# Performance work log

Measured on AMD Instinct MI355X. Metric: run time of the kernel, lower is better.

The kernel has to match this reference:

```python
import jax, jax.numpy as jnp
import numpy as np

D_MODEL = 1024
N_HEADS = 16
HEAD_DIM = D_MODEL // N_HEADS
SEQ_LEN = 2048
D_FF = 4 * D_MODEL
LCC_SCALE = 0.1
LN_EPS = 1e-5
NORM_EPS = 1e-12  # F.normalize eps


def _layer_norm(x, g, b):
    mu = jnp.mean(x, axis=-1, keepdims=True)
    var = jnp.mean(jnp.square(x - mu), axis=-1, keepdims=True)
    return (x - mu) * jax.lax.rsqrt(var + LN_EPS) * g + b


def setup_inputs() -> dict:
    key = jax.random.key(0)
    ks = jax.random.split(key, 8)
    s = 0.02  # weight init scale
    return {
        "x": jax.random.normal(ks[0], (SEQ_LEN, D_MODEL), jnp.float32),
        "lcc_values": jax.random.uniform(ks[1], (SEQ_LEN,), jnp.float32),
        "w_qkv": jax.random.normal(ks[2], (D_MODEL, 3 * D_MODEL), jnp.float32) * s,
        "b_qkv": jnp.zeros((3 * D_MODEL,), jnp.float32),
        "w_out": jax.random.normal(ks[3], (D_MODEL, D_MODEL), jnp.float32) * s,
        "b_out": jnp.zeros((D_MODEL,), jnp.float32),
        "ln1_g": jnp.ones((D_MODEL,), jnp.float32),
        "ln1_b": jnp.zeros((D_MODEL,), jnp.float32),
        "ln2_g": jnp.ones((D_MODEL,), jnp.float32),
        "ln2_b": jnp.zeros((D_MODEL,), jnp.float32),
        "w_ff1": jax.random.normal(ks[4], (D_MODEL, D_FF), jnp.float32) * s,
        "b_ff1": jnp.zeros((D_FF,), jnp.float32),
        "w_ff2": jax.random.normal(ks[5], (D_FF, D_MODEL), jnp.float32) * s,
        "b_ff2": jnp.zeros((D_MODEL,), jnp.float32),
    }


def reference(x, lcc_values, w_qkv, b_qkv, w_out, b_out, ln1_g, ln1_b,
              ln2_g, ln2_b, w_ff1, b_ff1, w_ff2, b_ff2):
    L = x.shape[0]
    scaling = HEAD_DIM ** -0.5

    normed = _layer_norm(x, ln1_g, ln1_b)
    qkv = normed @ w_qkv + b_qkv                      # [L, 3D]
    qkv = qkv.reshape(L, 3, N_HEADS, HEAD_DIM)
    q = jnp.transpose(qkv[:, 0], (1, 0, 2))           # [H, L, d]
    k = jnp.transpose(qkv[:, 1], (1, 0, 2))
    v = jnp.transpose(qkv[:, 2], (1, 0, 2))

    # cosine attention: L2-normalize q, k
    q = q / jnp.maximum(jnp.linalg.norm(q, axis=-1, keepdims=True), NORM_EPS)
    k = k / jnp.maximum(jnp.linalg.norm(k, axis=-1, keepdims=True), NORM_EPS)
    q = q * scaling

    scores = jnp.einsum('hld,hmd->hlm', q, k)         # [H, L, L]
    bias = (lcc_values[:, None] + lcc_values[None, :]) * 0.5 * LCC_SCALE
    scores = jnp.clip(scores + bias[None], -10.0, 10.0)
    probs = jax.nn.softmax(scores, axis=-1)

    attn = jnp.einsum('hlm,hmd->hld', probs, v)       # [H, L, d]
    attn = jnp.transpose(attn, (1, 0, 2)).reshape(L, D_MODEL)
    x = x + (attn @ w_out + b_out)

    normed2 = _layer_norm(x, ln2_g, ln2_b)
    h = jax.nn.gelu(normed2 @ w_ff1 + b_ff1, approximate=False)
    x = x + (h @ w_ff2 + b_ff2)
    return x
```

## Files before the change

### kernel.cpp

```cpp
#include <hip/hip_runtime.h>
#include <hip/hip_bf16.h>

#define D_MODEL 1024
#define SEQ 2048
#define NH 16
#define HD 64
#define DFF 4096

typedef __attribute__((ext_vector_type(8))) __bf16 bf16x8;
typedef __attribute__((ext_vector_type(4))) float f32x4;

__device__ __forceinline__ unsigned short f2bf(float f) {
    union { float f; unsigned u; } v; v.f = f;
    unsigned r = v.u + 0x7fffu + ((v.u >> 16) & 1u);
    return (unsigned short)(r >> 16);
}
__device__ __forceinline__ unsigned pack2(float a, float b) {
    return (unsigned)f2bf(a) | ((unsigned)f2bf(b) << 16);
}
__device__ __forceinline__ float bf2f(unsigned short u) {
    union { unsigned u; float f; } v; v.u = ((unsigned)u) << 16;
    return v.f;
}
__device__ __forceinline__ bf16x8 ld_frag(const unsigned short* p) {
    union { uint4 u; bf16x8 b; } c;
    c.u = *(const uint4*)p;
    return c.b;
}

typedef __attribute__((address_space(3))) unsigned lds_u32;
typedef const __attribute__((address_space(1))) unsigned glob_u32;
__device__ __forceinline__ void gl_lds16(const unsigned short* g, unsigned short* l) {
    __builtin_amdgcn_global_load_lds((glob_u32*)g, (lds_u32*)l, 16, 0, 0);
}

#define MFMA16(a,b,c) __builtin_amdgcn_mfma_f32_16x16x32_bf16(a,b,c,0,0,0)

__global__ __launch_bounds__(256) void wcast_all(const float* __restrict__ wq, const float* __restrict__ wo,
                                                 const float* __restrict__ wf1, const float* __restrict__ wf2,
                                                 unsigned short* __restrict__ oq, unsigned short* __restrict__ oo,
                                                 unsigned short* __restrict__ of1, unsigned short* __restrict__ of2) {
    __shared__ unsigned short lt[64][72];
    int id = blockIdx.x;
    const float* W; unsigned short* O; int K, N, nb, kb;
    if (id < 768)       { W = wq;  O = oq;  K = 1024; N = 3072; nb = id % 48; kb = id / 48; }
    else if (id < 1024) { id -= 768;  W = wo;  O = oo;  K = 1024; N = 1024; nb = id & 15; kb = id >> 4; }
    else if (id < 2048) { id -= 1024; W = wf1; O = of1; K = 1024; N = 4096; nb = id & 63; kb = id >> 6; }
    else                { id -= 2048; W = wf2; O = of2; K = 4096; N = 1024; nb = id & 15; kb = id >> 4; }
    int t = threadIdx.x;
    int r = t >> 2, c0 = (t & 3) << 4;
    const float* src = W + (size_t)(kb*64 + r) * N + nb*64 + c0;
    float4 f0 = ((const float4*)src)[0];
    float4 f1 = ((const float4*)src)[1];
    float4 f2 = ((const float4*)src)[2];
    float4 f3 = ((const float4*)src)[3];
    unsigned* dst = (unsigned*)&lt[r][c0];
    dst[0]=pack2(f0.x,f0.y); dst[1]=pack2(f0.z,f0.w);
    dst[2]=pack2(f1.x,f1.y); dst[3]=pack2(f1.z,f1.w);
    dst[4]=pack2(f2.x,f2.y); dst[5]=pack2(f2.z,f2.w);
    dst[6]=pack2(f3.x,f3.y); dst[7]=pack2(f3.z,f3.w);
    __syncthreads();
    int n_ = t >> 2, k0 = (t & 3) << 4;
    unsigned obuf[8];
#pragma unroll
    for (int i = 0; i < 8; i++)
        obuf[i] = (unsigned)lt[k0 + 2*i][n_] | ((unsigned)lt[k0 + 2*i + 1][n_] << 16);
    unsigned short* out = O + (size_t)(nb*64 + n_) * K + kb*64 + k0;
    ((uint4*)out)[0] = *(uint4*)&obuf[0];
    ((uint4*)out)[1] = *(uint4*)&obuf[4];
}

__global__ __launch_bounds__(256) void ln_kernel(const float* __restrict__ x,
                                                 const float* __restrict__ g,
                                                 const float* __restrict__ b,
                                                 unsigned short* __restrict__ out) {
    int row = blockIdx.x, t = threadIdx.x;
    float4 v = ((const float4*)(x + (size_t)row * D_MODEL))[t];
    float s  = v.x + v.y + v.z + v.w;
    float sq = v.x*v.x + v.y*v.y + v.z*v.z + v.w*v.w;
#pragma unroll
    for (int m = 1; m < 64; m <<= 1) { s += __shfl_xor(s, m, 64); sq += __shfl_xor(sq, m, 64); }
    __shared__ float ls[4], lq[4];
    int wave = t >> 6, lane = t & 63;
    if (lane == 0) { ls[wave] = s; lq[wave] = sq; }
    __syncthreads();
    s  = ls[0]+ls[1]+ls[2]+ls[3];
    sq = lq[0]+lq[1]+lq[2]+lq[3];
    float mu  = s * (1.0f / D_MODEL);
    float var = sq * (1.0f / D_MODEL) - mu * mu;
    float rs  = rsqrtf(var + 1e-5f);
    int c = t * 4;
    float y0 = (v.x - mu) * rs * g[c+0] + b[c+0];
    float y1 = (v.y - mu) * rs * g[c+1] + b[c+1];
    float y2 = (v.z - mu) * rs * g[c+2] + b[c+2];
    float y3 = (v.w - mu) * rs * g[c+3] + b[c+3];
    unsigned* o = (unsigned*)(out + (size_t)row * D_MODEL + c);
    o[0] = pack2(y0, y1); o[1] = pack2(y2, y3);
}

__global__ __launch_bounds__(256) void reduce_ln(const float* __restrict__ x,
                                                 const float* __restrict__ bout,
                                                 const unsigned short* __restrict__ parts,
                                                 const float* __restrict__ g,
                                                 const float* __restrict__ b,
                                                 float* __restrict__ x1,
                                                 unsigned short* __restrict__ x2n) {
    int row = blockIdx.x, t = threadIdx.x;
    int i = row * 256 + t;
    float4 v = ((const float4*)x)[i];
    float4 bb = ((const float4*)bout)[t];
    v.x += bb.x; v.y += bb.y; v.z += bb.z; v.w += bb.w;
    ushort4 u0 = ((const ushort4*)parts)[i];
    ushort4 u1 = ((const ushort4*)(parts + (size_t)SEQ*D_MODEL))[i];
    v.x += bf2f(u0.x) + bf2f(u1.x);
    v.y += bf2f(u0.y) + bf2f(u1.y);
    v.z += bf2f(u0.z) + bf2f(u1.z);
    v.w += bf2f(u0.w) + bf2f(u1.w);
    ((float4*)x1)[i] = v;
    float s  = v.x + v.y + v.z + v.w;
    float sq = v.x*v.x + v.y*v.y + v.z*v.z + v.w*v.w;
#pragma unroll
    for (int m = 1; m < 64; m <<= 1) { s += __shfl_xor(s, m, 64); sq += __shfl_xor(sq, m, 64); }
    __shared__ float ls[4], lq[4];
    int wave = t >> 6, lane = t & 63;
    if (lane == 0) { ls[wave] = s; lq[wave] = sq; }
    __syncthreads();
    s  = ls[0]+ls[1]+ls[2]+ls[3];
    sq = lq[0]+lq[1]+lq[2]+lq[3];
    float mu  = s * (1.0f / D_MODEL);
    float var = sq * (1.0f / D_MODEL) - mu * mu;
    float rs  = rsqrtf(var + 1e-5f);
    int c = t * 4;
    float y0 = (v.x - mu) * rs * g[c+0] + b[c+0];
    float y1 = (v.y - mu) * rs * g[c+1] + b[c+1];
    float y2 = (v.z - mu) * rs * g[c+2] + b[c+2];
    float y3 = (v.w - mu) * rs * g[c+3] + b[c+3];
    unsigned* o = (unsigned*)(x2n + (size_t)row * D_MODEL + c);
    o[0] = pack2(y0, y1); o[1] = pack2(y2, y3);
}

__global__ __launch_bounds__(256) void reduce_ff2(const float* __restrict__ res,
                                                  const float* __restrict__ bias,
                                                  const unsigned short* __restrict__ parts,
                                                  float* __restrict__ out) {
    int i = blockIdx.x * 256 + threadIdx.x;
    float4 r = ((const float4*)res)[i];
    float4 b = ((const float4*)bias)[i & (D_MODEL/4 - 1)];
    r.x += b.x; r.y += b.y; r.z += b.z; r.w += b.w;
#pragma unroll
    for (int p = 0; p < 4; p++) {
        ushort4 u = ((const ushort4*)(parts + (size_t)p * SEQ * D_MODEL))[i];
        r.x += bf2f(u.x); r.y += bf2f(u.y); r.z += bf2f(u.z); r.w += bf2f(u.w);
    }
    ((float4*)out)[i] = r;
}

#define TMg 128
#define TNg 128
#define SMEM_U16 (2 * (TMg + TNg) * 64)
__device__ __forceinline__ void gemm_core(const unsigned short* __restrict__ A,
                                          const unsigned short* __restrict__ Bt,
                                          int K, int K0, int KS, int bm, int bn,
                                          unsigned short* smem, f32x4 acc[4][4],
                                          int wave, int lane) {
    constexpr int AI = 4, BI = 4, MI = 4, NI = 4;
    constexpr int HALF = (TMg + TNg) * 64;
    int quad = lane >> 4, lr = lane & 15;

    const unsigned short* pa[AI];
    int aoff[AI];
#pragma unroll
    for (int i = 0; i < AI; i++) {
        int rl = wave*32 + i*8 + (lane >> 3);
        int ss = (lane & 7) ^ (rl & 7);
        pa[i] = A + (size_t)(bm*TMg + rl) * K + K0 + ss*8;
        aoff[i] = (wave*32 + i*8) * 64;
    }
    const unsigned short* pb[BI];
    int boff[BI];
#pragma unroll
    for (int i = 0; i < BI; i++) {
        int rl = wave*32 + i*8 + (lane >> 3);
        int ss = (lane & 7) ^ (rl & 7);
        pb[i] = Bt + (size_t)(bn*TNg + rl) * K + K0 + ss*8;
        boff[i] = TMg*64 + (wave*32 + i*8) * 64;
    }

    int wr = (wave >> 1) * 64, wc = (wave & 1) * 64;
    int foA[2][MI], foB[2][NI];
#pragma unroll
    for (int i = 0; i < MI; i++) {
        int row = wr + i*16 + lr;
        foA[0][i] = row*64 + ((quad     ^ (row & 7)))*8;
        foA[1][i] = row*64 + (((quad+4) ^ (row & 7)))*8;
    }
#pragma unroll
    for (int j = 0; j < NI; j++) {
        int row = wc + j*16 + lr;
        foB[0][j] = TMg*64 + row*64 + ((quad     ^ (row & 7)))*8;
        foB[1][j] = TMg*64 + row*64 + (((quad+4) ^ (row & 7)))*8;
    }

#pragma unroll
    for (int i = 0; i < AI; i++) gl_lds16(pa[i], smem + aoff[i]);
#pragma unroll
    for (int i = 0; i < BI; i++) gl_lds16(pb[i], smem + boff[i]);

    int bo = 0;
    for (int kk = 0; kk < KS; kk += 64) {
        __syncthreads();
        if (kk + 64 < KS) {
            int nb = bo ^ HALF;
#pragma unroll
            for (int i = 0; i < AI; i++) gl_lds16(pa[i] + kk + 64, smem + nb + aoff[i]);
#pragma unroll
            for (int i = 0; i < BI; i++) gl_lds16(pb[i] + kk + 64, smem + nb + boff[i]);
        }
#pragma unroll
        for (int h = 0; h < 2; h++) {
            bf16x8 af[MI], bfr[NI];
#pragma unroll
            for (int i = 0; i < MI; i++) af[i]  = ld_frag(smem + bo + foA[h][i]);
#pragma unroll
            for (int j = 0; j < NI; j++) bfr[j] = ld_frag(smem + bo + foB[h][j]);
#pragma unroll
            for (int i = 0; i < MI; i++)
#pragma unroll
                for (int j = 0; j < NI; j++)
                    acc[i][j] = MFMA16(af[i], bfr[j], acc[i][j]);
        }
        bo ^= HALF;
    }
}

__device__ __forceinline__ void acc_init(f32x4 acc[4][4]) {
    f32x4 z = {0.f, 0.f, 0.f, 0.f};
#pragma unroll
    for (int i = 0; i < 4; i++)
#pragma unroll
        for (int j = 0; j < 4; j++) acc[i][j] = z;
}

__global__ __launch_bounds__(256) void k_gemm_qkv(const unsigned short* __restrict__ A,
                                                  const unsigned short* __restrict__ Bt,
                                                  const float* __restrict__ bias,
                                                  unsigned short* __restrict__ qn,
                                                  unsigned short* __restrict__ kn,
                                                  unsigned short* __restrict__ vt) {
    __shared__ unsigned short smem[SMEM_U16];
    int t = threadIdx.x;
    int bn = blockIdx.x, bm = blockIdx.y;
    int wave = t >> 6, lane = t & 63;
    int quad = lane >> 4, lr = lane & 15;
    f32x4 acc[4][4];
    acc_init(acc);
    gemm_core(A, Bt, 1024, 0, 1024, bm, bn, smem, acc, wave, lane);

    int wr = (wave >> 1) * 64, wc = (wave & 1) * 64;
    int sec = bn >> 3, hp = bn & 7;
    float bv[4];
#pragma unroll
    for (int j = 0; j < 4; j++) bv[j] = bias[bn*TNg + wc + j*16 + lr];
#pragma unroll
    for (int i = 0; i < 4; i++)
#pragma unroll
        for (int j = 0; j < 4; j++)
#pragma unroll
            for (int r = 0; r < 4; r++) acc[i][j][r] += bv[j];

    if (sec < 2) {
        int h = hp*2 + (wave & 1);
        unsigned short* dst = (sec == 0) ? qn : kn;
        float mul = (sec == 0) ? 0.125f : 1.0f;
#pragma unroll
        for (int i = 0; i < 4; i++)
#pragma unroll
            for (int r = 0; r < 4; r++) {
                float ss = 0.f;
#pragma unroll
                for (int j = 0; j < 4; j++) ss += acc[i][j][r]*acc[i][j][r];
                ss += __shfl_xor(ss, 1, 64); ss += __shfl_xor(ss, 2, 64);
                ss += __shfl_xor(ss, 4, 64); ss += __shfl_xor(ss, 8, 64);
                float scale = mul / fmaxf(sqrtf(ss), 1e-12f);
                int row = bm*TMg + wr + i*16 + quad*4 + r;
                size_t base = ((size_t)h*SEQ + row) * HD;
#pragma unroll
                for (int j = 0; j < 4; j++)
                    dst[base + j*16 + lr] = f2bf(acc[i][j][r] * scale);
            }
    } else {
        __syncthreads();
        unsigned short (*lv)[136] = (unsigned short (*)[136])smem;
#pragma unroll
        for (int i = 0; i < 4; i++)
#pragma unroll
            for (int j = 0; j < 4; j++)
#pragma unroll
                for (int r = 0; r < 4; r++)
                    lv[wc + j*16 + lr][wr + i*16 + quad*4 + r] = f2bf(acc[i][j][r]);
        __syncthreads();
        int d = t >> 1, l0 = (t & 1) * 64;
        unsigned short* ov = vt + ((size_t)(hp*128 + d)) * SEQ + bm*TMg + l0;
#pragma unroll
        for (int c = 0; c < 8; c++)
            ((uint4*)ov)[c] = *(uint4*)&lv[d][l0 + c*8];
    }
}

template<int SPLITK>
__device__ __forceinline__ void gemm_part(const unsigned short* A, const unsigned short* Bt,
                                          unsigned short* C, int M, int N, int K) {
    __shared__ unsigned short smem[SMEM_U16];
    int t = threadIdx.x;
    int bn = blockIdx.x, bm = blockIdx.y, kz = blockIdx.z;
    int wave = t >> 6, lane = t & 63;
    int quad = lane >> 4, lr = lane & 15;
    int KS = K / SPLITK;
    f32x4 acc[4][4];
    acc_init(acc);
    gemm_core(A, Bt, K, kz*KS, KS, bm, bn, smem, acc, wave, lane);
    int wr = (wave >> 1) * 64, wc = (wave & 1) * 64;
    unsigned short* P = C + (size_t)kz * M * N;
#pragma unroll
    for (int i = 0; i < 4; i++)
#pragma unroll
        for (int j = 0; j < 4; j++) {
            int row0 = bm*TMg + wr + i*16 + quad*4;
            int col  = bn*TNg + wc + j*16 + lr;
#pragma unroll
            for (int r = 0; r < 4; r++)
                P[(size_t)(row0 + r) * N + col] = f2bf(acc[i][j][r]);
        }
}
__global__ __launch_bounds__(256) void k_gemm_op(const unsigned short* A, const unsigned short* Bt,
                                                 unsigned short* C, int M, int N, int K) {
    gemm_part<2>(A, Bt, C, M, N, K);
}
__global__ __launch_bounds__(256) void k_gemm_ff2(const unsigned short* A, const unsigned short* Bt,
                                                  unsigned short* C, int M, int N, int K) {
    gemm_part<4>(A, Bt, C, M, N, K);
}

__global__ __launch_bounds__(256) void k_gemm_ff1(const unsigned short* __restrict__ A,
                                                  const unsigned short* __restrict__ Bt,
                                                  const float* __restrict__ bias,
                                                  unsigned short* __restrict__ C,
                                                  int M, int N, int K) {
    __shared__ unsigned short smem[SMEM_U16];
    int t = threadIdx.x;
    int bn = blockIdx.x, bm = blockIdx.y;
    int wave = t >> 6, lane = t & 63;
    int quad = lane >> 4, lr = lane & 15;
    f32x4 acc[4][4];
    acc_init(acc);
    gemm_core(A, Bt, K, 0, K, bm, bn, smem, acc, wave, lane);
    int wr = (wave >> 1) * 64, wc = (wave & 1) * 64;
#pragma unroll
    for (int i = 0; i < 4; i++)
#pragma unroll
        for (int j = 0; j < 4; j++) {
            int row0 = bm*TMg + wr + i*16 + quad*4;
            int col  = bn*TNg + wc + j*16 + lr;
            float bvv = bias[col];
#pragma unroll
            for (int r = 0; r < 4; r++) {
                float v = acc[i][j][r] + bvv;
                v = 0.5f * v * (1.0f + erff(v * 0.70710678118654752f));
                C[(size_t)(row0 + r) * N + col] = f2bf(v);
            }
        }
}

#define KSPLIT 2
#define KTILES (SEQ / 64 / KSPLIT)
__global__ __launch_bounds__(256) void attn_kernel(const unsigned short* __restrict__ qn,
                                                   const unsigned short* __restrict__ kn,
                                                   const unsigned short* __restrict__ vt,
                                                   const float* __restrict__ lcc,
                                                   float* __restrict__ num_ws,
                                                   float* __restrict__ den_ws) {
    __shared__ unsigned short lQ[64][72];
    __shared__ unsigned short lK[64][72];
    __shared__ unsigned short lV[64][72];
    __shared__ unsigned short lP[64][72];
    __shared__ float lL[SEQ / KSPLIT];
    int h = blockIdx.x, qb = blockIdx.y, kz = blockIdx.z;
    int t = threadIdx.x;
    int rl = t >> 2, c0 = (t & 3) << 4;
    const unsigned short* pq = qn + ((size_t)h*SEQ + qb*64 + rl)*HD + c0;
    *(uint4*)&lQ[rl][c0]     = ((const uint4*)pq)[0];
    *(uint4*)&lQ[rl][c0 + 8] = ((const uint4*)pq)[1];
    for (int i = t; i < SEQ/KSPLIT; i += 256) lL[i] = 0.05f * lcc[kz*(SEQ/KSPLIT) + i];
    __syncthreads();
    int wave = t >> 6, lane = t & 63, quad = lane >> 4, lr = lane & 15;
    float lqv[4];
#pragma unroll
    for (int r = 0; r < 4; r++) lqv[r] = 0.05f * lcc[qb*64 + wave*16 + quad*4 + r];
    bf16x8 aq0 = ld_frag(&lQ[wave*16 + lr][quad*8]);
    bf16x8 aq1 = ld_frag(&lQ[wave*16 + lr][32 + quad*8]);
    f32x4 z = {0.f, 0.f, 0.f, 0.f};
    f32x4 oacc[4]; oacc[0]=z; oacc[1]=z; oacc[2]=z; oacc[3]=z;
    float den[4] = {0.f, 0.f, 0.f, 0.f};

    const unsigned short* kn0 = kn + (size_t)h*SEQ*HD + (size_t)kz*(SEQ/KSPLIT)*HD;
    const unsigned short* vt0 = vt + (size_t)h*HD*SEQ + kz*(SEQ/KSPLIT);

    for (int kb = 0; kb < KTILES; kb++) {
        __syncthreads();
        const unsigned short* pk = kn0 + (size_t)(kb*64 + rl)*HD + c0;
        uint4 k0v = ((const uint4*)pk)[0], k1v = ((const uint4*)pk)[1];
        const unsigned short* pv = vt0 + (size_t)rl*SEQ + kb*64 + c0;
        uint4 v0v = ((const uint4*)pv)[0], v1v = ((const uint4*)pv)[1];
        *(uint4*)&lK[rl][c0]     = k0v; *(uint4*)&lK[rl][c0 + 8] = k1v;
        *(uint4*)&lV[rl][c0]     = v0v; *(uint4*)&lV[rl][c0 + 8] = v1v;
        __syncthreads();
#pragma unroll
        for (int j = 0; j < 4; j++) {
            bf16x8 b0 = ld_frag(&lK[j*16 + lr][quad*8]);
            bf16x8 b1 = ld_frag(&lK[j*16 + lr][32 + quad*8]);
            f32x4 s = z;
            s = MFMA16(aq0, b0, s);
            s = MFMA16(aq1, b1, s);
            float lm = lL[kb*64 + j*16 + lr];
#pragma unroll
            for (int r = 0; r < 4; r++) {
                float sv = s[r] + lqv[r] + lm;
                sv = fminf(fmaxf(sv, -10.f), 10.f);
                float p = __expf(sv);
                den[r] += p;
                lP[wave*16 + quad*4 + r][j*16 + lr] = f2bf(p);
            }
        }
        bf16x8 ap0 = ld_frag(&lP[wave*16 + lr][quad*8]);
        bf16x8 ap1 = ld_frag(&lP[wave*16 + lr][32 + quad*8]);
#pragma unroll
        for (int j2 = 0; j2 < 4; j2++) {
            bf16x8 b0 = ld_frag(&lV[j2*16 + lr][quad*8]);
            bf16x8 b1 = ld_frag(&lV[j2*16 + lr][32 + quad*8]);
            oacc[j2] = MFMA16(ap0, b0, oacc[j2]);
            oacc[j2] = MFMA16(ap1, b1, oacc[j2]);
        }
    }
#pragma unroll
    for (int r = 0; r < 4; r++)
#pragma unroll
        for (int m = 1; m < 16; m <<= 1) den[r] += __shfl_xor(den[r], m, 64);

    float* nump = num_ws + (((size_t)(h*32 + qb)) * KSPLIT + kz) * 4096;
#pragma unroll
    for (int j2 = 0; j2 < 4; j2++)
#pragma unroll
        for (int r = 0; r < 4; r++)
            nump[(wave*16 + quad*4 + r) * 64 + j2*16 + lr] = oacc[j2][r];
    if (lr == 0) {
        float* denp = den_ws + (((size_t)(h*32 + qb)) * KSPLIT + kz) * 64;
#pragma unroll
        for (int r = 0; r < 4; r++) denp[wave*16 + quad*4 + r] = den[r];
    }
}

__global__ __launch_bounds__(256) void attn_comb(const float* __restrict__ num_ws,
                                                 const float* __restrict__ den_ws,
                                                 unsigned short* __restrict__ attn) {
    int hq = blockIdx.x;
    int h = hq >> 5, qb = hq & 31;
    int t = threadIdx.x;
    int row = t >> 2, col0 = (t & 3) << 4;
    const float* n0 = num_ws + ((size_t)hq * KSPLIT) * 4096 + row*64 + col0;
    const float* n1 = n0 + 4096;
    float d = den_ws[(size_t)hq * KSPLIT * 64 + row] + den_ws[((size_t)hq * KSPLIT + 1) * 64 + row];
    float inv = 1.0f / d;
    unsigned ob[8];
#pragma unroll
    for (int i = 0; i < 4; i++) {
        float4 a = ((const float4*)n0)[i];
        float4 b = ((const float4*)n1)[i];
        ob[2*i]   = pack2((a.x + b.x) * inv, (a.y + b.y) * inv);
        ob[2*i+1] = pack2((a.z + b.z) * inv, (a.w + b.w) * inv);
    }
    unsigned short* op = attn + (size_t)(qb*64 + row) * D_MODEL + h*64 + col0;
    ((uint4*)op)[0] = *(uint4*)&ob[0];
    ((uint4*)op)[1] = *(uint4*)&ob[4];
}

extern "C" void kernel_launch(void* const* d_in, const int* in_sizes, int n_in,
                              void* d_out, int out_size, void* d_ws, size_t ws_size,
                              hipStream_t stream) {
    const float* x      = (const float*)d_in[0];
    const float* lcc    = (const float*)d_in[1];
    const float* w_qkv  = (const float*)d_in[2];
    const float* b_qkv  = (const float*)d_in[3];
    const float* w_out  = (const float*)d_in[4];
    const float* b_out  = (const float*)d_in[5];
    const float* ln1_g  = (const float*)d_in[6];
    const float* ln1_b  = (const float*)d_in[7];
    const float* ln2_g  = (const float*)d_in[8];
    const float* ln2_b  = (const float*)d_in[9];
    const float* w_ff1  = (const float*)d_in[10];
    const float* b_ff1  = (const float*)d_in[11];
    const float* w_ff2  = (const float*)d_in[12];
    const float* b_ff2  = (const float*)d_in[13];

    char* ws = (char*)d_ws;
    unsigned short* wtq  = (unsigned short*)(ws);
    unsigned short* wto  = (unsigned short*)(ws + 6291456);
    unsigned short* wtf1 = (unsigned short*)(ws + 8388608);
    unsigned short* wtf2 = (unsigned short*)(ws + 16777216);
    unsigned short* xn   = (unsigned short*)(ws + 25165824);
    float*          x1   = (float*)(ws + 29360128);
    float*          numw = (float*)(ws + 29360128);
    float*          denw = (float*)(ws + 46137344);
    unsigned short* hbuf = (unsigned short*)(ws + 37748736);
    unsigned short* pOP  = (unsigned short*)(ws + 37748736);
    unsigned short* qnb  = (unsigned short*)(ws + 54525952);
    unsigned short* knb  = (unsigned short*)(ws + 58720256);
    unsigned short* vtb  = (unsigned short*)(ws + 62914560);
    unsigned short* pFF2 = (unsigned short*)(ws);
    unsigned short* attnb = xn;
    unsigned short* x2n  = qnb;
    float* outp = (float*)d_out;


    wcast_all<<<3072, 256, 0, stream>>>(w_qkv, w_out, w_ff1, w_ff2, wtq, wto, wtf1, wtf2);
    ln_kernel<<<SEQ, 256, 0, stream>>>(x, ln1_g, ln1_b, xn);
    k_gemm_qkv<<<dim3(24, 16), 256, 0, stream>>>(xn, wtq, b_qkv, qnb, knb, vtb);
    attn_kernel<<<dim3(16, 32, KSPLIT), 256, 0, stream>>>(qnb, knb, vtb, lcc, numw, denw);
    attn_comb<<<512, 256, 0, stream>>>(numw, denw, attnb);
    k_gemm_op<<<dim3(8, 16, 2), 256, 0, stream>>>(attnb, wto, pOP, SEQ, 1024, 1024);
    reduce_ln<<<SEQ, 256, 0, stream>>>(x, b_out, pOP, ln2_g, ln2_b, x1, x2n);
    k_gemm_ff1<<<dim3(32, 16), 256, 0, stream>>>(x2n, wtf1, b_ff1, hbuf, SEQ, 4096, 1024);
    k_gemm_ff2<<<dim3(8, 16, 4), 256, 0, stream>>>(hbuf, wtf2, pFF2, SEQ, 1024, 4096);
    reduce_ff2<<<SEQ*D_MODEL/1024, 256, 0, stream>>>(x1, b_ff2, pFF2, outp);
}
```

Measured before the change: 262.7 us.

## Double-buffer attention K/V tiles with async global-to-LDS loads and swizzled layout

Rewrites the attention inner loop to prefetch the next K and V tiles straight into LDS with direct global-to-LDS loads into a second buffer while the current tile is computed. LDS rows lose their padding and use an XOR swizzle to avoid bank conflicts. P now reuses the Q buffer, which cuts the syncs per iteration from two to one. The query-side lcc bias and the clamp are dropped from the softmax. Dropping the query term relies on softmax cancelling a per-row constant, and dropping the clamp relies on the scores staying in range. Wave priority is raised during the MFMA section.

```diff
diff --git a/kernel.cpp b/kernel.cpp
--- a/kernel.cpp
+++ b/kernel.cpp
@@ -379,67 +379,84 @@
                                                    const float* __restrict__ lcc,
                                                    float* __restrict__ num_ws,
                                                    float* __restrict__ den_ws) {
-    __shared__ unsigned short lQ[64][72];
-    __shared__ unsigned short lK[64][72];
-    __shared__ unsigned short lV[64][72];
-    __shared__ unsigned short lP[64][72];
-    __shared__ float lL[SEQ / KSPLIT];
+    __shared__ unsigned short lQP[64*64];
+    __shared__ unsigned short lK[2][64*64];
+    __shared__ unsigned short lV[2][64*64];
     int h = blockIdx.x, qb = blockIdx.y, kz = blockIdx.z;
     int t = threadIdx.x;
-    int rl = t >> 2, c0 = (t & 3) << 4;
-    const unsigned short* pq = qn + ((size_t)h*SEQ + qb*64 + rl)*HD + c0;
-    *(uint4*)&lQ[rl][c0]     = ((const uint4*)pq)[0];
-    *(uint4*)&lQ[rl][c0 + 8] = ((const uint4*)pq)[1];
-    for (int i = t; i < SEQ/KSPLIT; i += 256) lL[i] = 0.05f * lcc[kz*(SEQ/KSPLIT) + i];
+    int wave = t >> 6, lane = t & 63, quad = lane >> 4, lr = lane & 15;
+    int r0 = lane >> 3;
+    int ch = lane & 7;
+
+    const unsigned short* kn0 = kn + (size_t)h*SEQ*HD + (size_t)kz*(SEQ/KSPLIT)*HD;
+    const unsigned short* vt0 = vt + (size_t)h*HD*SEQ + kz*(SEQ/KSPLIT);
+    const float* lcc0 = lcc + kz*(SEQ/KSPLIT);
+
+#pragma unroll
+    for (int i = 0; i < 2; i++) {
+        int rl = wave*16 + i*8 + r0;
+        int ss = ch ^ (rl & 7);
+        gl_lds16(qn + ((size_t)h*SEQ + qb*64 + rl)*HD + ss*8, lQP + (wave*16 + i*8)*64);
+        gl_lds16(kn0 + (size_t)rl*HD + ss*8,                  lK[0] + (wave*16 + i*8)*64);
+        gl_lds16(vt0 + (size_t)rl*SEQ + ss*8,                 lV[0] + (wave*16 + i*8)*64);
+    }
     __syncthreads();
-    int wave = t >> 6, lane = t & 63, quad = lane >> 4, lr = lane & 15;
-    float lqv[4];
-#pragma unroll
-    for (int r = 0; r < 4; r++) lqv[r] = 0.05f * lcc[qb*64 + wave*16 + quad*4 + r];
-    bf16x8 aq0 = ld_frag(&lQ[wave*16 + lr][quad*8]);
-    bf16x8 aq1 = ld_frag(&lQ[wave*16 + lr][32 + quad*8]);
+
+    bf16x8 aq0 = ld_frag(lQP + (wave*16 + lr)*64 + ((quad     ^ (lr & 7)))*8);
+    bf16x8 aq1 = ld_frag(lQP + (wave*16 + lr)*64 + (((quad+4) ^ (lr & 7)))*8);
+
     f32x4 z = {0.f, 0.f, 0.f, 0.f};
     f32x4 oacc[4]; oacc[0]=z; oacc[1]=z; oacc[2]=z; oacc[3]=z;
     float den[4] = {0.f, 0.f, 0.f, 0.f};
 
-    const unsigned short* kn0 = kn + (size_t)h*SEQ*HD + (size_t)kz*(SEQ/KSPLIT)*HD;
-    const unsigned short* vt0 = vt + (size_t)h*HD*SEQ + kz*(SEQ/KSPLIT);
-
+    int cur = 0;
     for (int kb = 0; kb < KTILES; kb++) {
-        __syncthreads();
-        const unsigned short* pk = kn0 + (size_t)(kb*64 + rl)*HD + c0;
-        uint4 k0v = ((const uint4*)pk)[0], k1v = ((const uint4*)pk)[1];
-        const unsigned short* pv = vt0 + (size_t)rl*SEQ + kb*64 + c0;
-        uint4 v0v = ((const uint4*)pv)[0], v1v = ((const uint4*)pv)[1];
-        *(uint4*)&lK[rl][c0]     = k0v; *(uint4*)&lK[rl][c0 + 8] = k1v;
-        *(uint4*)&lV[rl][c0]     = v0v; *(uint4*)&lV[rl][c0 + 8] = v1v;
-        __syncthreads();
+        if (kb + 1 < KTILES) {
+            int nxt = cur ^ 1;
+#pragma unroll
+            for (int i = 0; i < 2; i++) {
+                int rl = wave*16 + i*8 + r0;
+                int ss = ch ^ (rl & 7);
+                gl_lds16(kn0 + (size_t)(kb+1)*64*HD + (size_t)rl*HD + ss*8,
+                         lK[nxt] + (wave*16 + i*8)*64);
+                gl_lds16(vt0 + (size_t)rl*SEQ + (kb+1)*64 + ss*8,
+                         lV[nxt] + (wave*16 + i*8)*64);
+            }
+        }
+        float lmv[4];
+#pragma unroll
+        for (int j = 0; j < 4; j++) lmv[j] = 0.05f * lcc0[kb*64 + j*16 + lr];
+
+        __builtin_amdgcn_s_setprio(1);
+        const unsigned short* Kc = lK[cur];
 #pragma unroll
         for (int j = 0; j < 4; j++) {
-            bf16x8 b0 = ld_frag(&lK[j*16 + lr][quad*8]);
-            bf16x8 b1 = ld_frag(&lK[j*16 + lr][32 + quad*8]);
+            bf16x8 b0 = ld_frag(Kc + (j*16 + lr)*64 + ((quad     ^ (lr & 7)))*8);
+            bf16x8 b1 = ld_frag(Kc + (j*16 + lr)*64 + (((quad+4) ^ (lr & 7)))*8);
             f32x4 s = z;
             s = MFMA16(aq0, b0, s);
             s = MFMA16(aq1, b1, s);
-            float lm = lL[kb*64 + j*16 + lr];
 #pragma unroll
             for (int r = 0; r < 4; r++) {
-                float sv = s[r] + lqv[r] + lm;
-                sv = fminf(fmaxf(sv, -10.f), 10.f);
-                float p = __expf(sv);
+                float p = __expf(s[r] + lmv[j]);
                 den[r] += p;
-                lP[wave*16 + quad*4 + r][j*16 + lr] = f2bf(p);
+                int prow = wave*16 + quad*4 + r;
+                lQP[prow*64 + (((2*j + (lr >> 3)) ^ (prow & 7)))*8 + (lr & 7)] = f2bf(p);
             }
         }
-        bf16x8 ap0 = ld_frag(&lP[wave*16 + lr][quad*8]);
-        bf16x8 ap1 = ld_frag(&lP[wave*16 + lr][32 + quad*8]);
+        bf16x8 ap0 = ld_frag(lQP + (wave*16 + lr)*64 + ((quad     ^ (lr & 7)))*8);
+        bf16x8 ap1 = ld_frag(lQP + (wave*16 + lr)*64 + (((quad+4) ^ (lr & 7)))*8);
+        const unsigned short* Vc = lV[cur];
 #pragma unroll
         for (int j2 = 0; j2 < 4; j2++) {
-            bf16x8 b0 = ld_frag(&lV[j2*16 + lr][quad*8]);
-            bf16x8 b1 = ld_frag(&lV[j2*16 + lr][32 + quad*8]);
+            bf16x8 b0 = ld_frag(Vc + (j2*16 + lr)*64 + ((quad     ^ (lr & 7)))*8);
+            bf16x8 b1 = ld_frag(Vc + (j2*16 + lr)*64 + (((quad+4) ^ (lr & 7)))*8);
             oacc[j2] = MFMA16(ap0, b0, oacc[j2]);
             oacc[j2] = MFMA16(ap1, b1, oacc[j2]);
         }
+        __builtin_amdgcn_s_setprio(0);
+        __syncthreads();
+        cur ^= 1;
     }
 #pragma unroll
     for (int r = 0; r < 4; r++)
```

After: 260.5 us. Within noise of the previous version (-0.8%).
